# Performance work log

Hardware: AMD Instinct MI355X
Metric: run time of the kernel (lower is better)

Reference implementation:

```python
import jax, jax.numpy as jnp
import numpy as np

N_G, E_G, E_LG = 32768, 131072, 262144
H, NODE_DIM, EDGE_DIM, NB, EB = 128, 32, 16, 4, 4
L, B, TASKS = 4, 256, 10
EPS_MSG = 1e-7   # GENConv message epsilon
BN_EPS = 1e-5    # eval-mode batchnorm (running_mean=0, running_var=1)


def setup_inputs() -> dict:
    key = jax.random.key(0)
    ks = jax.random.split(key, 24)
    s = 0.05
    inp = {
        'x_g': jax.random.normal(ks[0], (N_G, NODE_DIM), jnp.float32),
        'edge_attr_g': jax.random.normal(ks[1], (E_G, EDGE_DIM), jnp.float32),
        'x_lg': jax.random.normal(ks[2], (E_G, NB), jnp.float32),
        'edge_dist_basis': jax.random.normal(ks[3], (E_G, NB), jnp.float32),
        'edge_attr_lg': jax.random.normal(ks[4], (E_LG, EB), jnp.float32),
        'edge_index_g': jax.random.randint(ks[5], (2, E_G), 0, N_G, jnp.int32),
        'edge_index_lg': jax.random.randint(ks[6], (2, E_LG), 0, E_G, jnp.int32),
        'batch_idx': jnp.sort(jax.random.randint(ks[7], (N_G,), 0, B, jnp.int32)),
        # parameters
        'W_enc': jax.random.normal(ks[8], (NODE_DIM, H), jnp.float32) * s,
        'b_enc': jnp.zeros((H,), jnp.float32),
        'W_msg': jax.random.normal(ks[9], (2 * H + EDGE_DIM + NB, H), jnp.float32) * s,
        'b_msg': jnp.zeros((H,), jnp.float32),
        'W_nb': jax.random.normal(ks[10], (NB, H), jnp.float32) * s,
        'b_nb': jnp.zeros((H,), jnp.float32),
        'W_eb': jax.random.normal(ks[11], (EB, H), jnp.float32) * s,
        'b_eb': jnp.zeros((H,), jnp.float32),
        'W_gcn': jax.random.normal(ks[12], (L, H, H), jnp.float32) * s,
        'b_gcn': jnp.zeros((L, H), jnp.float32),
        't_vals': jnp.ones((L,), jnp.float32),
        'gamma': jnp.ones((L, H), jnp.float32) + 0.1 * jax.random.normal(ks[13], (L, H), jnp.float32),
        'beta': 0.1 * jax.random.normal(ks[14], (L, H), jnp.float32),
        'W_pred': jax.random.normal(ks[15], (H, TASKS), jnp.float32) * s,
        'b_pred': jnp.zeros((TASKS,), jnp.float32),
    }
    return inp


def _forward(x_g, edge_attr_g, x_lg, edge_dist_basis, edge_attr_lg,
             W_enc, b_enc, W_msg, b_msg, W_nb, b_nb, W_eb, b_eb,
             W_gcn, b_gcn, t_vals, gamma, beta, W_pred, b_pred,
             edge_index_g, edge_index_lg, batch_idx):
    # node encode + build initial per-edge (line-graph node) message embedding
    h_node = x_g @ W_enc + b_enc                              # [N_g, H]
    src_g, dst_g = edge_index_g[0], edge_index_g[1]
    msg_cat = jnp.concatenate(
        [h_node[src_g], h_node[dst_g], edge_attr_g, x_lg], axis=-1)
    h = msg_cat @ W_msg + b_msg                               # [E_g, H]

    nb = edge_dist_basis @ W_nb + b_nb                        # [E_g, H] dist basis emb
    eb = edge_attr_lg @ W_eb + b_eb                           # [E_lg, H] angle basis emb
    src, dst = edge_index_lg[0], edge_index_lg[1]
    n_lg = h.shape[0]

    def genconv(x, W, b, t):
        # message: source msg gated by dist basis of source edge and angle basis
        m = jax.nn.relu(x[src] * nb[src] * eb) + EPS_MSG       # [E_lg, H]
        s = m * t
        mx = jax.ops.segment_max(s, dst, num_segments=n_lg)
        ex = jnp.exp(s - mx[dst])
        den = jax.ops.segment_sum(ex, dst, num_segments=n_lg)
        num = jax.ops.segment_sum(ex * m, dst, num_segments=n_lg)
        agg = num / jnp.where(den > 0, den, 1.0)               # softmax aggregation
        return (x + agg) @ W + b                               # 1-layer MLP update

    inv = 1.0 / jnp.sqrt(jnp.float32(1.0 + BN_EPS))

    def bn(x, g, bt):  # eval-mode BN with running stats (0, 1)
        return x * (inv * g) + bt

    h = genconv(h, W_gcn[0], b_gcn[0], t_vals[0])
    for l in range(1, L):  # res+ blocks (dropout off in eval)
        h2 = jax.nn.relu(bn(h, gamma[l - 1], beta[l - 1]))
        h = genconv(h2, W_gcn[l], b_gcn[l], t_vals[l]) + h
    h = bn(h, gamma[L - 1], beta[L - 1])

    node_emb = jax.ops.segment_sum(h, dst_g, num_segments=N_G)  # scatter_add back
    counts = jax.ops.segment_sum(jnp.ones((N_G,), h.dtype), batch_idx, num_segments=B)
    gsum = jax.ops.segment_sum(node_emb, batch_idx, num_segments=B)
    h_graph = gsum / jnp.maximum(counts, 1.0)[:, None]           # mean pool
    return h_graph @ W_pred + b_pred


def reference(x_g, edge_attr_g, x_lg, edge_dist_basis, edge_attr_lg,
              W_enc, b_enc, W_msg, b_msg, W_nb, b_nb, W_eb, b_eb,
              W_gcn, b_gcn, t_vals, gamma, beta, W_pred, b_pred,
              edge_index_g, edge_index_lg, batch_idx):
    return _forward(x_g, edge_attr_g, x_lg, edge_dist_basis, edge_attr_lg,
                    W_enc, b_enc, W_msg, b_msg, W_nb, b_nb, W_eb, b_eb,
                    W_gcn, b_gcn, t_vals, gamma, beta, W_pred, b_pred,
                    edge_index_g, edge_index_lg, batch_idx)
```

## Files before the change

kernel.cpp:

```cpp
#include <hip/hip_runtime.h>

typedef unsigned short u16;
typedef __attribute__((ext_vector_type(4))) float f32x4;
typedef __attribute__((ext_vector_type(8))) short short8;

#define N_G_   32768
#define E_G_   131072
#define E_LG_  262144
#define H_     128
#define B_     256
#define TASKS_ 10
#define KPAD_  288
#define LDST_  296
#define CPAD_  132
#define APAD_  136
#define INVBN_ 0.9999950000374997f
#define NCVT_  20
#define TOTAL_CANON_ 5352216

__device__ __forceinline__ float bf2f(u16 h){
  union { unsigned int u; float f; } v; v.u = ((unsigned int)h) << 16; return v.f;
}
__device__ __forceinline__ u16 f2bf(float f){
  union { float f; unsigned int u; } v; v.f = f;
  unsigned int u = v.u + 0x7fffu + ((v.u >> 16) & 1u);
  return (u16)(u >> 16);
}

__global__ void k_detect(const unsigned int* __restrict__ x, int* __restrict__ flag){
  __shared__ int sm[256];
  unsigned int v = x[threadIdx.x];
  unsigned int e = (v >> 7) & 0xFFu;
  sm[threadIdx.x] = (e >= 110u && e <= 140u) ? 1 : 0;
  __syncthreads();
  for (int s=128;s>0;s>>=1){ if (threadIdx.x < s) sm[threadIdx.x] += sm[threadIdx.x+s]; __syncthreads(); }
  if (threadIdx.x == 0) flag[0] = (sm[0] > 128) ? 1 : 0;
}

struct CvtArgs { const void* src[NCVT_]; int start[NCVT_]; int count[NCVT_]; };

__global__ void k_cvt(CvtArgs a, int total, const int* __restrict__ flag, u16* __restrict__ dst){
  int i = blockIdx.x*256 + threadIdx.x;
  if (i >= total) return;
  int s = 0;
  #pragma unroll
  for (int j=1;j<NCVT_;j++) if (i >= a.start[j]) s = j;
  int off = i - a.start[s];
  if (off >= a.count[s]) { dst[i] = 0; return; }
  if (flag[0]) dst[i] = ((const u16*)a.src[s])[off];
  else         dst[i] = f2bf(((const float*)a.src[s])[off]);
}

__global__ void k_pack(const u16* __restrict__ Wg, const u16* __restrict__ Wm,
                       u16* __restrict__ WTg, u16* __restrict__ WTm){
  int idx = blockIdx.x*256 + threadIdx.x;
  if (idx < 4*128*128){
    int l = idx >> 14, n = (idx >> 7) & 127, k = idx & 127;
    WTg[idx] = Wg[((l<<7) + k)*128 + n];
  }
  if (idx < 128*KPAD_){
    int n = idx / KPAD_, kp = idx % KPAD_;
    WTm[idx] = (kp < 276) ? Wm[kp*128 + n] : (u16)0;
  }
}

__global__ __launch_bounds__(256) void k_enc(const u16* __restrict__ xg, const u16* __restrict__ We,
                      const u16* __restrict__ be, u16* __restrict__ hn){
  int idx = blockIdx.x*256 + threadIdx.x;
  int r = idx >> 7, c = idx & 127;
  float acc = bf2f(be[c]);
  const u16* xr = xg + r*32;
  #pragma unroll
  for (int k=0;k<32;k++) acc += bf2f(xr[k]) * bf2f(We[k*128 + c]);
  hn[idx] = f2bf(acc);
}

__global__ __launch_bounds__(256) void k_msg(const u16* __restrict__ hn, const u16* __restrict__ eag,
     const u16* __restrict__ xlg, const int* __restrict__ eig,
     const u16* __restrict__ WTm, const u16* __restrict__ bmsg, u16* __restrict__ h){
  __shared__ __align__(16) u16 As[64*LDST_];
  int tid = threadIdx.x;
  int e0 = blockIdx.x * 64;
  {
    int i = tid >> 2;
    int j = tid & 3;
    int e = e0 + i;
    int s = eig[e];
    int d = eig[E_G_ + e];
    u16* rowp = As + i*LDST_;
    const u16* ps = hn + s*128 + j*32;
    const u16* pd = hn + d*128 + j*32;
    #pragma unroll
    for (int q=0;q<4;q++) *(short8*)(rowp + j*32 + q*8)       = *(const short8*)(ps + q*8);
    #pragma unroll
    for (int q=0;q<4;q++) *(short8*)(rowp + 128 + j*32 + q*8) = *(const short8*)(pd + q*8);
    if (j == 0){
      *(short8*)(rowp + 256) = *(const short8*)(eag + e*16);
      *(short8*)(rowp + 264) = *(const short8*)(eag + e*16 + 8);
      *(ushort4*)(rowp + 272) = *(const ushort4*)(xlg + e*4);
      *(ushort4*)(rowp + 276) = (ushort4){0,0,0,0};
      *(short8*)(rowp + 280) = (short8){0,0,0,0,0,0,0,0};
    }
  }
  __syncthreads();
  int wave = tid >> 6, lane = tid & 63, quad = lane >> 4, l16 = lane & 15;
  int arow = wave*16 + l16;
  f32x4 acc[8];
  #pragma unroll
  for (int ct=0;ct<8;ct++) acc[ct] = (f32x4){0.f,0.f,0.f,0.f};
  for (int ks=0; ks<KPAD_; ks+=32){
    short8 af = *(const short8*)(As + arow*LDST_ + ks + quad*8);
    #pragma unroll
    for (int ct=0;ct<8;ct++){
      short8 bfr = *(const short8*)(WTm + (ct*16 + l16)*KPAD_ + ks + quad*8);
      acc[ct] = __builtin_amdgcn_mfma_f32_16x16x32_bf16(af, bfr, acc[ct], 0,0,0);
    }
  }
  __syncthreads();
  float* Cs = (float*)As;
  {
    int lrow = wave*16 + quad*4;
    #pragma unroll
    for (int ct=0;ct<8;ct++){
      int col = ct*16 + l16;
      #pragma unroll
      for (int i=0;i<4;i++) Cs[(lrow+i)*CPAD_ + col] = acc[ct][i];
    }
  }
  __syncthreads();
  #pragma unroll
  for (int p=0;p<4;p++){
    int s = p*256 + tid;
    int lrow = s >> 4, c0 = (s & 15) * 8;
    const float* cp = Cs + lrow*CPAD_ + c0;
    short8 bs = *(const short8*)(bmsg + c0);
    short8 ov;
    #pragma unroll
    for (int k=0;k<8;k++) ov[k] = (short)f2bf(cp[k] + bf2f((u16)bs[k]));
    *(short8*)(h + (size_t)(e0 + lrow)*128 + c0) = ov;
  }
}

__global__ __launch_bounds__(256) void k_agg_gemm(
    const u16* __restrict__ ht, const int2* __restrict__ pairs, const int* __restrict__ off,
    const u16* __restrict__ w, const u16* __restrict__ tvals, int layer,
    const u16* __restrict__ WT, const u16* __restrict__ bg,
    u16* __restrict__ h, int residual,
    const u16* __restrict__ gamma, const u16* __restrict__ beta,
    u16* __restrict__ h2, int write_h2){
  __shared__ __align__(16) float Cs[16*CPAD_];
  u16* As = (u16*)Cs;
  int tid = threadIdx.x;
  int e0 = blockIdx.x*16;

  {
    int r = tid >> 4;
    int c0 = (tid & 15) * 8;
    int g = e0 + r;
    float t = bf2f(tvals[layer]);
    float den[8]={0.f,0.f,0.f,0.f,0.f,0.f,0.f,0.f};
    float num[8]={0.f,0.f,0.f,0.f,0.f,0.f,0.f,0.f};
    int kb = off[g], ke = off[g+1];
    for (int k=kb; k<ke; k++){
      int src = pairs[k].x;
      short8 xu = *(const short8*)(ht + (size_t)src*128 + c0);
      short8 wu = *(const short8*)(w + (size_t)k*128 + c0);
      #pragma unroll
      for (int j=0;j<8;j++){
        float m  = fmaxf(bf2f((u16)xu[j])*bf2f((u16)wu[j]), 0.f) + 1e-7f;
        float e1 = __expf(m*t);
        den[j] += e1;
        num[j] = fmaf(e1, m, num[j]);
      }
    }
    short8 xdu = *(const short8*)(ht + (size_t)g*128 + c0);
    short8 ov;
    #pragma unroll
    for (int j=0;j<8;j++)
      ov[j] = (short)f2bf(bf2f((u16)xdu[j]) + (den[j] > 0.f ? num[j]/den[j] : 0.f));
    *(short8*)(As + r*APAD_ + c0) = ov;
  }
  __syncthreads();

  int wave = tid >> 6, lane = tid & 63, quad = lane >> 4, l16 = lane & 15;
  f32x4 acc[2];
  acc[0] = (f32x4){0.f,0.f,0.f,0.f};
  acc[1] = (f32x4){0.f,0.f,0.f,0.f};
  #pragma unroll
  for (int ks=0;ks<128;ks+=32){
    short8 af = *(const short8*)(As + l16*APAD_ + ks + quad*8);
    #pragma unroll
    for (int c2=0;c2<2;c2++){
      int ct = wave*2 + c2;
      short8 bfr = *(const short8*)(WT + (ct*16 + l16)*128 + ks + quad*8);
      acc[c2] = __builtin_amdgcn_mfma_f32_16x16x32_bf16(af, bfr, acc[c2], 0,0,0);
    }
  }
  __syncthreads();
  {
    int lrow = quad*4;
    #pragma unroll
    for (int c2=0;c2<2;c2++){
      int col = (wave*2 + c2)*16 + l16;
      #pragma unroll
      for (int i=0;i<4;i++) Cs[(lrow+i)*CPAD_ + col] = acc[c2][i];
    }
  }
  __syncthreads();

  {
    int lrow = tid >> 4, c0 = (tid & 15) * 8;
    const float* cp = Cs + lrow*CPAD_ + c0;
    size_t goff = (size_t)(e0 + lrow)*128 + c0;
    short8 bs = *(const short8*)(bg + c0);
    float v[8];
    #pragma unroll
    for (int k=0;k<8;k++) v[k] = cp[k] + bf2f((u16)bs[k]);
    if (residual){
      short8 hs = *(const short8*)(h + goff);
      #pragma unroll
      for (int k=0;k<8;k++) v[k] += bf2f((u16)hs[k]);
    }
    short8 ov;
    #pragma unroll
    for (int k=0;k<8;k++) ov[k] = (short)f2bf(v[k]);
    *(short8*)(h + goff) = ov;
    if (write_h2){
      short8 gs = *(const short8*)(gamma + layer*128 + c0);
      short8 es = *(const short8*)(beta  + layer*128 + c0);
      short8 o2;
      #pragma unroll
      for (int k=0;k<8;k++)
        o2[k] = (short)f2bf(fmaxf(fmaf(v[k], bf2f((u16)gs[k])*INVBN_, bf2f((u16)es[k])), 0.f));
      *(short8*)(h2 + goff) = o2;
    }
  }
}

__global__ void k_count(const int* __restrict__ dst, int n, int* __restrict__ cnt){
  int i = blockIdx.x*256 + threadIdx.x;
  if (i < n) atomicAdd(&cnt[dst[i]], 1);
}
__global__ void k_bsum(const int* __restrict__ cnt, int n, int* __restrict__ bsum){
  __shared__ int sm[256];
  int i = blockIdx.x*256 + threadIdx.x;
  sm[threadIdx.x] = (i < n) ? cnt[i] : 0;
  __syncthreads();
  for (int s=128;s>0;s>>=1){ if (threadIdx.x < s) sm[threadIdx.x] += sm[threadIdx.x+s]; __syncthreads(); }
  if (threadIdx.x==0) bsum[blockIdx.x] = sm[0];
}
__global__ void k_scanb(const int* __restrict__ bsum, int nb, int* __restrict__ bbase,
                        int* __restrict__ off, int n){
  __shared__ int sm[1024];
  int t = threadIdx.x;
  int v = (t < nb) ? bsum[t] : 0;
  sm[t] = v; __syncthreads();
  for (int d=1; d<1024; d<<=1){
    int u = (t>=d) ? sm[t-d] : 0;
    __syncthreads();
    sm[t] += u;
    __syncthreads();
  }
  if (t < nb) bbase[t] = sm[t] - v;
  if (t == 1023) off[n] = sm[1023];
}
__global__ void k_offsets(const int* __restrict__ cnt, const int* __restrict__ bbase,
                          int* __restrict__ off, int n){
  __shared__ int sm[256];
  int i = blockIdx.x*256 + threadIdx.x;
  int t = threadIdx.x;
  int v = (i < n) ? cnt[i] : 0;
  sm[t] = v; __syncthreads();
  for (int d=1; d<256; d<<=1){
    int u = (t>=d) ? sm[t-d] : 0;
    __syncthreads();
    sm[t] += u;
    __syncthreads();
  }
  if (i < n) off[i] = bbase[blockIdx.x] + sm[t] - v;
}
__global__ void k_scatter_lg(const int* __restrict__ eilg, const int* __restrict__ off,
                             int* __restrict__ cur, int2* __restrict__ pairs){
  int e = blockIdx.x*256 + threadIdx.x;
  if (e >= E_LG_) return;
  int s = eilg[e], d = eilg[E_LG_ + e];
  int p = off[d] + atomicAdd(&cur[d], 1);
  pairs[p] = make_int2(s, e);
}
__global__ void k_scatter_g(const int* __restrict__ eig, const int* __restrict__ off2,
                            int* __restrict__ cur2, int* __restrict__ eids){
  int e = blockIdx.x*256 + threadIdx.x;
  if (e >= E_G_) return;
  int d = eig[E_G_ + e];
  int p = off2[d] + atomicAdd(&cur2[d], 1);
  eids[p] = e;
}

__global__ __launch_bounds__(256) void k_wprep(const int2* __restrict__ pairs,
    const u16* __restrict__ dbas, const u16* __restrict__ ealg,
    const u16* __restrict__ Wnb, const u16* __restrict__ bnb,
    const u16* __restrict__ Web, const u16* __restrict__ beb,
    u16* __restrict__ w){
  int c0 = (threadIdx.x & 15) * 8;
  float wnb[4][8], web[4][8], vbn[8], vbe[8];
  #pragma unroll
  for (int i=0;i<4;i++){
    short8 a = *(const short8*)(Wnb + i*128 + c0);
    short8 b = *(const short8*)(Web + i*128 + c0);
    #pragma unroll
    for (int j=0;j<8;j++){ wnb[i][j]=bf2f((u16)a[j]); web[i][j]=bf2f((u16)b[j]); }
  }
  {
    short8 a = *(const short8*)(bnb + c0);
    short8 b = *(const short8*)(beb + c0);
    #pragma unroll
    for (int j=0;j<8;j++){ vbn[j]=bf2f((u16)a[j]); vbe[j]=bf2f((u16)b[j]); }
  }
  int g0 = blockIdx.x*16 + (threadIdx.x >> 4);
  int gs = gridDim.x*16;
  for (int p = g0; p < E_LG_; p += gs){
    int2 pr = pairs[p];
    ushort4 du = *(const ushort4*)(dbas + pr.x*4);
    ushort4 eu = *(const ushort4*)(ealg + pr.y*4);
    float db[4] = {bf2f(du.x), bf2f(du.y), bf2f(du.z), bf2f(du.w)};
    float ev[4] = {bf2f(eu.x), bf2f(eu.y), bf2f(eu.z), bf2f(eu.w)};
    short8 ov;
    #pragma unroll
    for (int j=0;j<8;j++){
      float nbv = vbn[j] + db[0]*wnb[0][j] + db[1]*wnb[1][j] + db[2]*wnb[2][j] + db[3]*wnb[3][j];
      float ebv = vbe[j] + ev[0]*web[0][j] + ev[1]*web[1][j] + ev[2]*web[2][j] + ev[3]*web[3][j];
      ov[j] = (short)f2bf(nbv * ebv);
    }
    *(short8*)(w + (size_t)p*128 + c0) = ov;
  }
}

__global__ __launch_bounds__(256) void k_pool_nodes(const u16* __restrict__ h, const int* __restrict__ off2,
    const int* __restrict__ eids,
    const u16* __restrict__ gamma, const u16* __restrict__ beta,
    float* __restrict__ node_emb){
  int tid = blockIdx.x*256 + threadIdx.x;
  int n = tid >> 5;
  int c0 = (tid & 31)*4;
  ushort4 ga = *(const ushort4*)(gamma + 3*128 + c0);
  ushort4 be = *(const ushort4*)(beta + 3*128 + c0);
  float gg[4] = {bf2f(ga.x)*INVBN_, bf2f(ga.y)*INVBN_, bf2f(ga.z)*INVBN_, bf2f(ga.w)*INVBN_};
  float bt[4] = {bf2f(be.x), bf2f(be.y), bf2f(be.z), bf2f(be.w)};
  float s[4] = {0.f,0.f,0.f,0.f};
  int kb = off2[n], ke = off2[n+1];
  for (int k=kb; k<ke; k++){
    int e = eids[k];
    ushort4 xu = *(const ushort4*)(h + (size_t)e*128 + c0);
    float xs[4] = {bf2f(xu.x), bf2f(xu.y), bf2f(xu.z), bf2f(xu.w)};
    #pragma unroll
    for (int j=0;j<4;j++) s[j] += fmaf(xs[j], gg[j], bt[j]);
  }
  f32x4 ov = {s[0], s[1], s[2], s[3]};
  *(f32x4*)(node_emb + (size_t)n*128 + c0) = ov;
}

__global__ __launch_bounds__(128) void k_poolpred(const float* __restrict__ node_emb,
    const int* __restrict__ bidx,
    const u16* __restrict__ Wp, const u16* __restrict__ bp,
    const int* __restrict__ flag, void* __restrict__ out){
  int b = blockIdx.x;
  int t = threadIdx.x;
  int lo = 0, hi_s = N_G_;
  { int l = 0, r = N_G_;
    while (l < r){ int m = (l+r)>>1; if (bidx[m] < b) l = m+1; else r = m; }
    lo = l;
    l = lo; r = N_G_;
    while (l < r){ int m = (l+r)>>1; if (bidx[m] < b+1) l = m+1; else r = m; }
    hi_s = l;
  }
  float s = 0.f;
  for (int n=lo; n<hi_s; n++) s += node_emb[(size_t)n*128 + t];
  __shared__ float sm[128];
  sm[t] = s;
  __syncthreads();
  if (t < TASKS_){
    float inv = 1.0f / fmaxf((float)(hi_s - lo), 1.0f);
    float acc = bf2f(bp[t]);
    #pragma unroll 4
    for (int c=0;c<128;c++) acc += sm[c]*inv * bf2f(Wp[c*TASKS_ + t]);
    if (flag[0]) ((u16*)out)[b*TASKS_ + t] = f2bf(acc);
    else         ((float*)out)[b*TASKS_ + t] = acc;
  }
}

extern "C" void kernel_launch(void* const* d_in, const int* in_sizes, int n_in,
                              void* d_out, int out_size, void* d_ws, size_t ws_size,
                              hipStream_t stream){
  const int* eig  = (const int*)d_in[5];
  const int* eilg = (const int*)d_in[6];
  const int* bidx = (const int*)d_in[7];

  char* ws = (char*)d_ws; size_t o = 0;
  auto carve = [&](size_t b)->char*{ char* p = ws + o; o += (b + 255) & ~(size_t)255; return p; };
  int*  flag  = (int*) carve(256);
  u16*  canon = (u16*) carve((size_t)TOTAL_CANON_*2);
  u16*  h     = (u16*) carve((size_t)E_G_*H_*2);
  u16*  h2    = (u16*) carve((size_t)E_G_*H_*2);
  u16*  hn    = (u16*) carve((size_t)N_G_*H_*2);
  u16*  WTg   = (u16*) carve((size_t)4*128*128*2);
  u16*  WTm   = (u16*) carve((size_t)128*KPAD_*2);
  int*  cnt1  = (int*) carve((size_t)E_G_*4);
  int*  off1  = (int*) carve((size_t)(E_G_+1)*4);
  int2* pairs = (int2*)carve((size_t)E_LG_*8);
  int*  cnt2  = (int*) carve((size_t)N_G_*4);
  int*  off2  = (int*) carve((size_t)(N_G_+1)*4);
  int*  eids  = (int*) carve((size_t)E_G_*4);
  int*  bsum  = (int*) carve(1024*4);
  int*  bbase = (int*) carve(1024*4);
  float* node_emb = (float*)carve((size_t)N_G_*H_*4);
  u16* w_sorted = (u16*)carve((size_t)E_LG_*H_*2);
  (void)in_sizes; (void)n_in; (void)out_size; (void)ws_size;

  static const int di[NCVT_] = {0,1,2,3,4, 8,9,10,11,12,13,14,15,16,17,18,19,20,21,22};
  static const int st[NCVT_] = {0,1048576,3145728,3670016,4194304,
                                5242880,5246976,5247104,5282432,5282560,
                                5283072,5283200,5283712,5283840,5349376,
                                5349888,5349896,5350408,5350920,5352200};
  static const int cn[NCVT_] = {1048576,2097152,524288,524288,1048576,
                                4096,128,35328,128,512,
                                128,512,128,65536,512,
                                4,512,512,1280,10};
  CvtArgs ca;
  for (int i=0;i<NCVT_;i++){ ca.src[i]=d_in[di[i]]; ca.start[i]=st[i]; ca.count[i]=cn[i]; }

  const u16* x_g   = canon + st[0];
  const u16* ea_g  = canon + st[1];
  const u16* x_lg  = canon + st[2];
  const u16* dbas  = canon + st[3];
  const u16* ea_lg = canon + st[4];
  const u16* W_enc = canon + st[5];
  const u16* b_enc = canon + st[6];
  const u16* W_msg = canon + st[7];
  const u16* b_msg = canon + st[8];
  const u16* W_nb  = canon + st[9];
  const u16* b_nb  = canon + st[10];
  const u16* W_eb  = canon + st[11];
  const u16* b_eb  = canon + st[12];
  const u16* W_gcn = canon + st[13];
  const u16* b_gcn = canon + st[14];
  const u16* t_vals= canon + st[15];
  const u16* gamma = canon + st[16];
  const u16* beta  = canon + st[17];
  const u16* W_pred= canon + st[18];
  const u16* b_pred= canon + st[19];

  k_detect<<<1,256,0,stream>>>((const unsigned int*)d_in[0], flag);
  k_cvt<<<(TOTAL_CANON_+255)/256,256,0,stream>>>(ca, TOTAL_CANON_, flag, canon);

  k_pack<<<256,256,0,stream>>>(W_gcn, W_msg, WTg, WTm);
  k_enc<<<N_G_*H_/256,256,0,stream>>>(x_g, W_enc, b_enc, hn);
  k_msg<<<E_G_/64,256,0,stream>>>(hn, ea_g, x_lg, eig, WTm, b_msg, h);

  hipMemsetAsync(cnt1, 0, (size_t)E_G_*4, stream);
  k_count<<<E_LG_/256,256,0,stream>>>(eilg + E_LG_, E_LG_, cnt1);
  k_bsum<<<E_G_/256,256,0,stream>>>(cnt1, E_G_, bsum);
  k_scanb<<<1,1024,0,stream>>>(bsum, E_G_/256, bbase, off1, E_G_);
  k_offsets<<<E_G_/256,256,0,stream>>>(cnt1, bbase, off1, E_G_);
  hipMemsetAsync(cnt1, 0, (size_t)E_G_*4, stream);
  k_scatter_lg<<<E_LG_/256,256,0,stream>>>(eilg, off1, cnt1, pairs);

  k_wprep<<<2048,256,0,stream>>>(pairs, dbas, ea_lg, W_nb, b_nb, W_eb, b_eb, w_sorted);

  hipMemsetAsync(cnt2, 0, (size_t)N_G_*4, stream);
  k_count<<<E_G_/256,256,0,stream>>>(eig + E_G_, E_G_, cnt2);
  k_bsum<<<N_G_/256,256,0,stream>>>(cnt2, N_G_, bsum);
  k_scanb<<<1,1024,0,stream>>>(bsum, N_G_/256, bbase, off2, N_G_);
  k_offsets<<<N_G_/256,256,0,stream>>>(cnt2, bbase, off2, N_G_);
  hipMemsetAsync(cnt2, 0, (size_t)N_G_*4, stream);
  k_scatter_g<<<E_G_/256,256,0,stream>>>(eig, off2, cnt2, eids);

  for (int l=0; l<4; l++){
    const u16* ht = (l == 0) ? h : h2;
    k_agg_gemm<<<E_G_/16,256,0,stream>>>(ht, pairs, off1, w_sorted, t_vals, l,
        WTg + (size_t)l*128*128, b_gcn + l*128, h, (l>0)?1:0,
        gamma, beta, h2, (l<3)?1:0);
  }

  k_pool_nodes<<<N_G_*32/256,256,0,stream>>>(h, off2, eids, gamma, beta, node_emb);
  k_poolpred<<<B_,128,0,stream>>>(node_emb, bidx, W_pred, b_pred, flag, d_out);
}
```

Baseline: 576.9 us.

## Balance edge aggregation across threads with shared-memory atomics and fuse BN into gather

The per-row gather loop, where each thread walked its own destination's incoming list (load imbalanced and serial), becomes a block-wide strided loop over all incoming pairs of the 16 rows. Partial num/den sums are accumulated with LDS float atomics using a new per-pair destination array. The batchnorm+ReLU for the residual input is now applied on the fly during the gather instead of materialising a separate h2 buffer, and h is ping-ponged between two buffers. This adds LDS atomic contention, a larger shared footprint, and recomputes BN per gathered element.

Result: slower. 1.882 ms (+226.2%).

```diff
diff --git a/kernel.cpp b/kernel.cpp
--- a/kernel.cpp
+++ b/kernel.cpp
@@ -142,42 +142,72 @@
 }
 
 __global__ __launch_bounds__(256) void k_agg_gemm(
-    const u16* __restrict__ ht, const int2* __restrict__ pairs, const int* __restrict__ off,
+    const u16* __restrict__ hin, const int2* __restrict__ pairs, const int* __restrict__ off,
+    const int* __restrict__ dstl,
     const u16* __restrict__ w, const u16* __restrict__ tvals, int layer,
     const u16* __restrict__ WT, const u16* __restrict__ bg,
-    u16* __restrict__ h, int residual,
     const u16* __restrict__ gamma, const u16* __restrict__ beta,
-    u16* __restrict__ h2, int write_h2){
-  __shared__ __align__(16) float Cs[16*CPAD_];
-  u16* As = (u16*)Cs;
+    u16* __restrict__ hout, int residual){
+  __shared__ __align__(16) float smemf[4096];
+  __shared__ __align__(16) u16 As[16*APAD_];
+  float* denS = smemf;
+  float* numS = smemf + 2048;
   int tid = threadIdx.x;
   int e0 = blockIdx.x*16;
 
   {
+    f32x4 z = {0.f,0.f,0.f,0.f};
+    #pragma unroll
+    for (int q=0;q<4;q++) *(f32x4*)(smemf + tid*16 + q*4) = z;
+  }
+  __syncthreads();
+
+  int c0 = (tid & 15) * 8;
+  float t = bf2f(tvals[layer]);
+  bool dobn = (layer > 0);
+  float gg[8], bb[8];
+  if (dobn){
+    short8 gs = *(const short8*)(gamma + (layer-1)*128 + c0);
+    short8 es = *(const short8*)(beta  + (layer-1)*128 + c0);
+    #pragma unroll
+    for (int j=0;j<8;j++){ gg[j] = bf2f((u16)gs[j])*INVBN_; bb[j] = bf2f((u16)es[j]); }
+  } else {
+    #pragma unroll
+    for (int j=0;j<8;j++){ gg[j] = 1.f; bb[j] = 0.f; }
+  }
+
+  int kb = off[e0], ke = off[e0+16];
+  for (int p = kb + (tid >> 4); p < ke; p += 16){
+    int2 pr = pairs[p];
+    int r = dstl[p] - e0;
+    short8 xu = *(const short8*)(hin + (size_t)pr.x*128 + c0);
+    short8 wu = *(const short8*)(w + (size_t)p*128 + c0);
+    float* dp = denS + r*128 + c0;
+    float* np = numS + r*128 + c0;
+    #pragma unroll
+    for (int j=0;j<8;j++){
+      float x = bf2f((u16)xu[j]);
+      if (dobn) x = fmaxf(fmaf(x, gg[j], bb[j]), 0.f);
+      float m  = fmaxf(x*bf2f((u16)wu[j]), 0.f) + 1e-7f;
+      float e1 = __expf(m*t);
+      atomicAdd(dp + j, e1);
+      atomicAdd(np + j, e1*m);
+    }
+  }
+  __syncthreads();
+
+  {
     int r = tid >> 4;
-    int c0 = (tid & 15) * 8;
     int g = e0 + r;
-    float t = bf2f(tvals[layer]);
-    float den[8]={0.f,0.f,0.f,0.f,0.f,0.f,0.f,0.f};
-    float num[8]={0.f,0.f,0.f,0.f,0.f,0.f,0.f,0.f};
-    int kb = off[g], ke = off[g+1];
-    for (int k=kb; k<ke; k++){
-      int src = pairs[k].x;
-      short8 xu = *(const short8*)(ht + (size_t)src*128 + c0);
-      short8 wu = *(const short8*)(w + (size_t)k*128 + c0);
-      #pragma unroll
-      for (int j=0;j<8;j++){
-        float m  = fmaxf(bf2f((u16)xu[j])*bf2f((u16)wu[j]), 0.f) + 1e-7f;
-        float e1 = __expf(m*t);
-        den[j] += e1;
-        num[j] = fmaf(e1, m, num[j]);
-      }
-    }
-    short8 xdu = *(const short8*)(ht + (size_t)g*128 + c0);
+    short8 xdu = *(const short8*)(hin + (size_t)g*128 + c0);
     short8 ov;
     #pragma unroll
-    for (int j=0;j<8;j++)
-      ov[j] = (short)f2bf(bf2f((u16)xdu[j]) + (den[j] > 0.f ? num[j]/den[j] : 0.f));
+    for (int j=0;j<8;j++){
+      float x = bf2f((u16)xdu[j]);
+      if (dobn) x = fmaxf(fmaf(x, gg[j], bb[j]), 0.f);
+      float dn = denS[r*128 + c0 + j];
+      ov[j] = (short)f2bf(x + (dn > 0.f ? numS[r*128 + c0 + j]/dn : 0.f));
+    }
     *(short8*)(As + r*APAD_ + c0) = ov;
   }
   __syncthreads();
@@ -196,7 +226,7 @@
       acc[c2] = __builtin_amdgcn_mfma_f32_16x16x32_bf16(af, bfr, acc[c2], 0,0,0);
     }
   }
-  __syncthreads();
+  float* Cs = smemf;
   {
     int lrow = quad*4;
     #pragma unroll
@@ -209,31 +239,22 @@
   __syncthreads();
 
   {
-    int lrow = tid >> 4, c0 = (tid & 15) * 8;
-    const float* cp = Cs + lrow*CPAD_ + c0;
-    size_t goff = (size_t)(e0 + lrow)*128 + c0;
-    short8 bs = *(const short8*)(bg + c0);
+    int lrow = tid >> 4, ce = (tid & 15) * 8;
+    const float* cp = Cs + lrow*CPAD_ + ce;
+    size_t goff = (size_t)(e0 + lrow)*128 + ce;
+    short8 bs = *(const short8*)(bg + ce);
     float v[8];
     #pragma unroll
     for (int k=0;k<8;k++) v[k] = cp[k] + bf2f((u16)bs[k]);
     if (residual){
-      short8 hs = *(const short8*)(h + goff);
+      short8 hs = *(const short8*)(hin + goff);
       #pragma unroll
       for (int k=0;k<8;k++) v[k] += bf2f((u16)hs[k]);
     }
     short8 ov;
     #pragma unroll
     for (int k=0;k<8;k++) ov[k] = (short)f2bf(v[k]);
-    *(short8*)(h + goff) = ov;
-    if (write_h2){
-      short8 gs = *(const short8*)(gamma + layer*128 + c0);
-      short8 es = *(const short8*)(beta  + layer*128 + c0);
-      short8 o2;
-      #pragma unroll
-      for (int k=0;k<8;k++)
-        o2[k] = (short)f2bf(fmaxf(fmaf(v[k], bf2f((u16)gs[k])*INVBN_, bf2f((u16)es[k])), 0.f));
-      *(short8*)(h2 + goff) = o2;
-    }
+    *(short8*)(hout + goff) = ov;
   }
 }
 
@@ -280,12 +301,14 @@
   if (i < n) off[i] = bbase[blockIdx.x] + sm[t] - v;
 }
 __global__ void k_scatter_lg(const int* __restrict__ eilg, const int* __restrict__ off,
-                             int* __restrict__ cur, int2* __restrict__ pairs){
+                             int* __restrict__ cur, int2* __restrict__ pairs,
+                             int* __restrict__ dstl){
   int e = blockIdx.x*256 + threadIdx.x;
   if (e >= E_LG_) return;
   int s = eilg[e], d = eilg[E_LG_ + e];
   int p = off[d] + atomicAdd(&cur[d], 1);
   pairs[p] = make_int2(s, e);
+  dstl[p] = d;
 }
 __global__ void k_scatter_g(const int* __restrict__ eig, const int* __restrict__ off2,
                             int* __restrict__ cur2, int* __restrict__ eids){
@@ -400,13 +423,14 @@
   int*  flag  = (int*) carve(256);
   u16*  canon = (u16*) carve((size_t)TOTAL_CANON_*2);
   u16*  h     = (u16*) carve((size_t)E_G_*H_*2);
-  u16*  h2    = (u16*) carve((size_t)E_G_*H_*2);
+  u16*  hb1   = (u16*) carve((size_t)E_G_*H_*2);
   u16*  hn    = (u16*) carve((size_t)N_G_*H_*2);
   u16*  WTg   = (u16*) carve((size_t)4*128*128*2);
   u16*  WTm   = (u16*) carve((size_t)128*KPAD_*2);
   int*  cnt1  = (int*) carve((size_t)E_G_*4);
   int*  off1  = (int*) carve((size_t)(E_G_+1)*4);
   int2* pairs = (int2*)carve((size_t)E_LG_*8);
+  int*  dstl  = (int*) carve((size_t)E_LG_*4);
   int*  cnt2  = (int*) carve((size_t)N_G_*4);
   int*  off2  = (int*) carve((size_t)(N_G_+1)*4);
   int*  eids  = (int*) carve((size_t)E_G_*4);
@@ -462,7 +486,7 @@
   k_scanb<<<1,1024,0,stream>>>(bsum, E_G_/256, bbase, off1, E_G_);
   k_offsets<<<E_G_/256,256,0,stream>>>(cnt1, bbase, off1, E_G_);
   hipMemsetAsync(cnt1, 0, (size_t)E_G_*4, stream);
-  k_scatter_lg<<<E_LG_/256,256,0,stream>>>(eilg, off1, cnt1, pairs);
+  k_scatter_lg<<<E_LG_/256,256,0,stream>>>(eilg, off1, cnt1, pairs, dstl);
 
   k_wprep<<<2048,256,0,stream>>>(pairs, dbas, ea_lg, W_nb, b_nb, W_eb, b_eb, w_sorted);
 
@@ -474,13 +498,14 @@
   hipMemsetAsync(cnt2, 0, (size_t)N_G_*4, stream);
   k_scatter_g<<<E_G_/256,256,0,stream>>>(eig, off2, cnt2, eids);
 
+  u16* hin = h;
+  u16* hout = hb1;
   for (int l=0; l<4; l++){
-    const u16* ht = (l == 0) ? h : h2;
-    k_agg_gemm<<<E_G_/16,256,0,stream>>>(ht, pairs, off1, w_sorted, t_vals, l,
-        WTg + (size_t)l*128*128, b_gcn + l*128, h, (l>0)?1:0,
-        gamma, beta, h2, (l<3)?1:0);
-  }
-
-  k_pool_nodes<<<N_G_*32/256,256,0,stream>>>(h, off2, eids, gamma, beta, node_emb);
+    k_agg_gemm<<<E_G_/16,256,0,stream>>>(hin, pairs, off1, dstl, w_sorted, t_vals, l,
+        WTg + (size_t)l*128*128, b_gcn + l*128, gamma, beta, hout, (l>0)?1:0);
+    u16* tmp = hin; hin = hout; hout = tmp;
+  }
+
+  k_pool_nodes<<<N_G_*32/256,256,0,stream>>>(hin, off2, eids, gamma, beta, node_emb);
   k_poolpred<<<B_,128,0,stream>>>(node_emb, bidx, W_pred, b_pred, flag, d_out);
 }
```
